# Kernel optimization log

Measured on AMD Instinct MI355X. Metric: run time of the kernel, lower is better.

The kernel has to match this reference:

```python
import jax, jax.numpy as jnp
import numpy as np

# B anchors, N neighbors, M views, F raw features, OBS router obs dim,
# D d_model, H heads, L layers, FF ffn dim, HID router hidden, OUT out_dim
B, N, M, F, OBS, D, H, L, FF, HID, OUT = 4096, 64, 4, 128, 64, 64, 4, 2, 128, 64, 8
EPS = 1e-6

def _ln(x, g, b):
    m = x.mean(-1, keepdims=True)
    v = ((x - m) ** 2).mean(-1, keepdims=True)
    return (x - m) / jnp.sqrt(v + 1e-5) * g + b

def _gelu(x):
    return jax.nn.gelu(x, approximate=False)

def setup_inputs() -> dict:
    key = jax.random.key(0)
    ks = iter(jax.random.split(key, 64))
    def nrm(shape, scale=0.05):
        return jax.random.normal(next(ks), shape, dtype=jnp.float32) * scale
    return dict(
        x_anc=jax.random.normal(next(ks), (B, F), dtype=jnp.float32),
        g_anc=jax.random.normal(next(ks), (B, OBS), dtype=jnp.float32),
        x_nei=jax.random.normal(next(ks), (B, N, F), dtype=jnp.float32),
        ew_anc=jax.random.uniform(next(ks), (B, N, M), dtype=jnp.float32),
        W_anc=nrm((F, D)), b_anc=jnp.zeros((D,), jnp.float32),
        Wv_emb=nrm((M, F, D)), bv_emb=jnp.zeros((M, D), jnp.float32),
        Wv_val=nrm((M, D, D)), bv_val=jnp.zeros((M, D), jnp.float32),
        r_Win=nrm((OBS + D, HID)), r_bin=jnp.zeros((HID,), jnp.float32),
        r_lng=jnp.ones((HID,), jnp.float32), r_lnb=jnp.zeros((HID,), jnp.float32),
        r_W1=nrm((HID, HID)), r_b1=jnp.zeros((HID,), jnp.float32),
        r_W2=nrm((HID, HID)), r_b2=jnp.zeros((HID,), jnp.float32),
        r_Wview=nrm((H, HID, M)), r_bview=jnp.zeros((H, M), jnp.float32),
        r_Wmode=nrm((H, HID)), r_bmode=jnp.zeros((H,), jnp.float32),
        log_tau=jnp.zeros((H,), jnp.float32),
        L_Wq=nrm((L, D, D)), L_Wk=nrm((L, D, D)), L_Wv=nrm((L, D, D)), L_Wo=nrm((L, D, D)),
        L_ln1g=jnp.ones((L, D), jnp.float32), L_ln1b=jnp.zeros((L, D), jnp.float32),
        L_ln2g=jnp.ones((L, D), jnp.float32), L_ln2b=jnp.zeros((L, D), jnp.float32),
        L_Wf1=nrm((L, D, FF)), L_bf1=jnp.zeros((L, FF), jnp.float32),
        L_Wf2=nrm((L, FF, D)), L_bf2=jnp.zeros((L, D), jnp.float32),
        p_lng=jnp.ones((D,), jnp.float32), p_lnb=jnp.zeros((D,), jnp.float32),
        p_W1=nrm((D, D // 2)), p_b1=jnp.zeros((D // 2,), jnp.float32),
        p_W2=nrm((D // 2, OUT)), p_b2=jnp.zeros((OUT,), jnp.float32),
    )

def reference(x_anc, g_anc, x_nei, ew_anc,
              W_anc, b_anc, Wv_emb, bv_emb, Wv_val, bv_val,
              r_Win, r_bin, r_lng, r_lnb, r_W1, r_b1, r_W2, r_b2,
              r_Wview, r_bview, r_Wmode, r_bmode, log_tau,
              L_Wq, L_Wk, L_Wv, L_Wo, L_ln1g, L_ln1b, L_ln2g, L_ln2b,
              L_Wf1, L_bf1, L_Wf2, L_bf2,
              p_lng, p_lnb, p_W1, p_b1, p_W2, p_b2):
    view_mask = (ew_anc > 0).astype(ew_anc.dtype)  # default view_mask
    # anchor / per-view neighbor embeddings
    h_anc = x_anc @ W_anc + b_anc                                    # [B,D]
    h_nei = jnp.einsum('bnf,mfd->bmnd', x_nei, Wv_emb) + bv_emb[None, :, None, :]  # [B,M,N,D]
    # per-view values + masked weight normalization + weighted neighbor sum
    vals = jnp.einsum('bmnd,mde->bmne', h_nei, Wv_val) + bv_val[None, :, None, :]
    w = (ew_anc * view_mask).transpose(0, 2, 1)                      # [B,M,N]
    w = w / jnp.clip(w.sum(-1, keepdims=True), EPS)
    per_view_ctx = jnp.einsum('bmn,bmnd->bmd', w, vals)              # [B,M,D]
    ctx_vec = per_view_ctx.mean(1)                                   # [B,D]
    iso_view_ctxs = per_view_ctx                                     # same masked reduce (no lbl_delta)
    # SplitTrackRouter
    h = jnp.concatenate([g_anc, ctx_vec], -1) @ r_Win + r_bin
    h = _gelu(_ln(h, r_lng, r_lnb))
    h = _gelu(h @ r_W1 + r_b1)
    h = _gelu(h @ r_W2 + r_b2)
    pi = jax.nn.softmax(jnp.einsum('bk,hkm->bhm', h, r_Wview) + r_bview, axis=-1)  # [B,H,M]
    beta = jax.nn.sigmoid(jnp.einsum('bk,hk->bh', h, r_Wmode) + r_bmode)           # [B,H]
    tau = jnp.exp(log_tau)                                                         # [H]
    iso_heads = jnp.einsum('bhm,bmd->bhd', pi, iso_view_ctxs)                      # [B,H,D]
    # SparseGeomLayer stack: anchor->neighbor cross attention gated by pi-weighted edge weights
    h_nei_shared = h_nei[:, 0]                                                     # [B,N,D]
    dh = D // H
    scale = 1.0 / (float(dh) ** 0.5)
    w_view = jnp.einsum('bhm,bnm->bhn', pi, ew_anc * view_mask)                    # [B,H,N]
    gate = jnp.log(w_view + EPS)
    x = h_anc
    for l in range(L):
        q = (x @ L_Wq[l]).reshape(B, H, dh)
        k = (h_nei_shared @ L_Wk[l]).reshape(B, N, H, dh)
        v = (h_nei_shared @ L_Wv[l]).reshape(B, N, H, dh)
        scores = jnp.einsum('bhd,bnhd->bhn', q, k) * scale / tau[None, :, None] + gate
        attn = jax.nn.softmax(scores, axis=-1)
        ctx = jnp.einsum('bhn,bnhd->bhd', attn, v).reshape(B, D) @ L_Wo[l]
        x = _ln(x + ctx, L_ln1g[l], L_ln1b[l])
        ff = _gelu(x @ L_Wf1[l] + L_bf1[l]) @ L_Wf2[l] + L_bf2[l]
        x = _ln(x + ff, L_ln2g[l], L_ln2b[l])
    # blend_iso_interaction
    blended = ((1.0 - beta)[..., None] * iso_heads + beta[..., None] * x[:, None, :]).mean(1)  # [B,D]
    # pred head
    y = _ln(blended, p_lng, p_lnb)
    y = _gelu(y @ p_W1 + p_b1) @ p_W2 + p_b2
    return y
```

## Files before the change

kernel.cpp:

```cpp
#include <hip/hip_runtime.h>
#include <hip/hip_bf16.h>
#include <math.h>

#define NB 4096
#define NN 64
#define NM 4
#define NF 128
#define NOBS 64
#define ND 64
#define NH 4
#define NLAYER 2
#define NFF 128
#define NHID 64
#define NOUT 8
#define EPSC 1e-6f

typedef unsigned short ushort_t;
typedef __attribute__((ext_vector_type(8))) short short8v;
typedef __attribute__((ext_vector_type(4))) float f32x4;

#define MFMA16(a, b, c) __builtin_amdgcn_mfma_f32_16x16x32_bf16((a), (b), (c), 0, 0, 0)

struct GParams {
    const float* x_anc; const float* g_anc; const float* x_nei; const float* ew_anc;
    const float* W_anc; const float* b_anc;
    const float* Wv_emb; const float* bv_emb; const float* Wv_val; const float* bv_val;
    const float* r_Win; const float* r_bin; const float* r_lng; const float* r_lnb;
    const float* r_W1; const float* r_b1; const float* r_W2; const float* r_b2;
    const float* r_Wview; const float* r_bview; const float* r_Wmode; const float* r_bmode;
    const float* log_tau;
    const float* L_Wq; const float* L_Wk; const float* L_Wv; const float* L_Wo;
    const float* L_ln1g; const float* L_ln1b; const float* L_ln2g; const float* L_ln2b;
    const float* L_Wf1; const float* L_bf1; const float* L_Wf2; const float* L_bf2;
    const float* p_lng; const float* p_lnb; const float* p_W1; const float* p_b1;
    const float* p_W2; const float* p_b2;
    const uint4* wsf;
    float* out;
};

__device__ __forceinline__ float gelu_f(float x) {
    return 0.5f * x * (1.0f + erff(x * 0.7071067811865476f));
}
__device__ __forceinline__ float wsum64(float v) {
#pragma unroll
    for (int off = 32; off > 0; off >>= 1) v += __shfl_xor(v, off, 64);
    return v;
}
__device__ __forceinline__ float wmax64(float v) {
#pragma unroll
    for (int off = 32; off > 0; off >>= 1) v = fmaxf(v, __shfl_xor(v, off, 64));
    return v;
}
__device__ __forceinline__ float bf2f(ushort_t u) {
    union { unsigned int i; float f; } c; c.i = ((unsigned int)u) << 16; return c.f;
}
__device__ __forceinline__ ushort_t f2bf(float f) {
    __hip_bfloat16 h = __float2bfloat16(f);
    ushort_t u; __builtin_memcpy(&u, &h, 2); return u;
}
__device__ __forceinline__ short8v ld_frag(const uint4* p) {
    union { uint4 q; short8v v; } u; u.q = *p; return u.v;
}

__global__ void prep_w(const float* Wv_emb, const float* L_Wk, const float* L_Wv, uint4* ws)
{
    int task = blockIdx.x * 256 + threadIdx.x;
    if (task >= 3072) return;
    int lane = task & 63;
    int frag = task >> 6;
    const float* src; int ks, ct; uint4 *dhi, *dlo;
    if (frag < 16) {
        ks = frag >> 2; ct = frag & 3;
        src = Wv_emb;
        dhi = ws + (size_t)frag * 64 + lane;
        dlo = ws + 1024 + (size_t)frag * 64 + lane;
    } else {
        int g = frag - 16;
        int matidx = g >> 3;
        int fi = g & 7;
        ks = fi >> 2; ct = fi & 3;
        src = ((matidx & 1) ? L_Wv : L_Wk) + (size_t)(matidx >> 1) * (ND * ND);
        dhi = ws + 2048 + (size_t)matidx * 1024 + (size_t)fi * 64 + lane;
        dlo = dhi + 512;
    }
    union { ushort_t u[8]; uint4 q; } hi, lo;
#pragma unroll
    for (int i = 0; i < 8; i++) {
        int k = ks * 32 + (lane >> 4) * 8 + i;
        int d = ct * 16 + (lane & 15);
        float w = src[k * ND + d];
        ushort_t h = f2bf(w);
        hi.u[i] = h;
        lo.u[i] = f2bf(w - bf2f(h));
    }
    *dhi = hi.q;
    *dlo = lo.q;
}

__global__ __launch_bounds__(256, 3)
void gora_fused(GParams P)
{
    const int b = blockIdx.x;
    const int t = threadIdx.x;
    const int lane = t & 63;
    const int wave = t >> 6;

    __shared__ alignas(16) char u1buf[NN * NF * 2];
    __shared__ float hv[NM][ND];
    __shared__ __hip_bfloat16 kb16[NN][ND + 2];
    __shared__ __hip_bfloat16 vb16[NN][ND + 2];
    __shared__ float ew_s[NN * NM];
    __shared__ float winv[NM], wssum[NM];
    __shared__ float xa[NF];
    __shared__ float ga[NOBS];
    __shared__ float xw[NM][NF];
    __shared__ float pvc[NM][ND];
    __shared__ float hfin[NHID];
    __shared__ float pi_raw[NH * NM];
    __shared__ float pi_s[NH][NM];
    __shared__ float beta_s[NH];
    __shared__ float gate_s[NH][NN];
    __shared__ float xcur[ND];
    __shared__ float qv[ND];
    __shared__ float attn_s[NH][NN];
    __shared__ float ctx_s[ND];
    __shared__ float ffs[NFF];
    __shared__ float sA[ND];
    __shared__ float sB[ND];

    {
        float e = P.ew_anc[(size_t)b * NN * NM + t];
        ew_s[t] = (e > 0.0f) ? e : 0.0f;
    }
    if (t < NF) xa[t] = P.x_anc[(size_t)b * NF + t];
    else if (t < NF + NOBS) ga[t - NF] = P.g_anc[(size_t)b * NOBS + (t - NF)];
    {
        const float4* xn4 = (const float4*)(P.x_nei + (size_t)b * NN * NF);
#pragma unroll
        for (int i = 0; i < 8; i++) {
            int i4 = t + i * 256;
            float4 v4 = xn4[i4];
            __hip_bfloat162 p0, p1;
            p0.x = __float2bfloat16(v4.x); p0.y = __float2bfloat16(v4.y);
            p1.x = __float2bfloat16(v4.z); p1.y = __float2bfloat16(v4.w);
            int n = i4 >> 5;
            int c = (i4 >> 1) & 15;
            char* dstb = u1buf + n * 256 + ((c ^ (n & 15)) << 4) + (i4 & 1) * 8;
            ((__hip_bfloat162*)dstb)[0] = p0;
            ((__hip_bfloat162*)dstb)[1] = p1;
        }
    }
    __syncthreads();

    if (t < NM) {
        float s = 0.0f;
        for (int n = 0; n < NN; n++) s += ew_s[n * NM + t];
        float c = fmaxf(s, EPSC);
        winv[t]  = 1.0f / c;
        wssum[t] = s / c;
    }
    if (t >= 64 && t < 128) {
        int d = t - 64;
        float acc = P.b_anc[d];
        for (int f = 0; f < NF; f++) acc += xa[f] * P.W_anc[f * ND + d];
        xcur[d] = acc;
    }
    __syncthreads();

    {
        int f = t & (NF - 1);
        int m0 = t >> 7;
        const char* base = u1buf + ((((f >> 3)) << 4)) * 0;
        float a0 = 0.f, a1 = 0.f;
        for (int n = 0; n < NN; n++) {
            const ushort_t* xp = (const ushort_t*)(u1buf + n * 256 + (((f >> 3) ^ (n & 15)) << 4) + (f & 7) * 2);
            float xv = bf2f(*xp);
            a0 += ew_s[n * NM + m0] * xv;
            a1 += ew_s[n * NM + m0 + 2] * xv;
        }
        xw[m0][f]     = a0 * winv[m0];
        xw[m0 + 2][f] = a1 * winv[m0 + 2];
    }

    short8v afr[4];
    {
        const int row = wave * 16 + (lane & 15);
        const int sub = lane >> 4;
#pragma unroll
        for (int ks = 0; ks < 4; ks++) {
            int c = ks * 4 + sub;
            afr[ks] = *(const short8v*)(u1buf + row * 256 + ((c ^ (row & 15)) << 4));
        }
    }
    __syncthreads();

    {
        const int n0 = wave * 16;
        const int colb = lane & 15;
        const int rsub = lane >> 4;
#pragma unroll
        for (int ct = 0; ct < 4; ct++) {
            float bias = P.bv_emb[ct * 16 + colb];
            f32x4 c = {bias, bias, bias, bias};
#pragma unroll
            for (int ks = 0; ks < 4; ks++) {
                short8v bhi = ld_frag(P.wsf + (size_t)(ks * 4 + ct) * 64 + lane);
                short8v blo = ld_frag(P.wsf + 1024 + (size_t)(ks * 4 + ct) * 64 + lane);
                c = MFMA16(afr[ks], bhi, c);
                c = MFMA16(afr[ks], blo, c);
            }
#pragma unroll
            for (int e = 0; e < 4; e++) {
                int n = n0 + rsub * 4 + e;
                int d = ct * 16 + colb;
                *(float*)(u1buf + n * 256 + ((((d >> 2) ^ (n & 15))) << 4) + (d & 3) * 4) = c[e];
            }
        }
    }

    {
        int m = wave, d = lane;
        float acc = wssum[m] * P.bv_emb[m * ND + d];
        const float* We = P.Wv_emb + (size_t)m * NF * ND;
        for (int f = 0; f < NF; f++) acc += xw[m][f] * We[f * ND + d];
        hv[m][d] = acc;
    }
    __syncthreads();
    {
        int m = wave, d = lane;
        float acc = wssum[m] * P.bv_val[m * ND + d];
        const float* Wv = P.Wv_val + (size_t)m * ND * ND;
        for (int k = 0; k < ND; k++) acc += hv[m][k] * Wv[k * ND + d];
        pvc[m][d] = acc;
    }
    __syncthreads();

    if (t < ND) sA[t] = 0.25f * (pvc[0][t] + pvc[1][t] + pvc[2][t] + pvc[3][t]);
    __syncthreads();
    if (t < NHID) {
        float acc = P.r_bin[t];
        for (int f = 0; f < NOBS; f++) acc += ga[f] * P.r_Win[f * NHID + t];
        for (int f = 0; f < ND;   f++) acc += sA[f] * P.r_Win[(NOBS + f) * NHID + t];
        float mean = wsum64(acc) * (1.0f / 64.0f);
        float dv = acc - mean;
        float var = wsum64(dv * dv) * (1.0f / 64.0f);
        float xln = dv * rsqrtf(var + 1e-5f) * P.r_lng[t] + P.r_lnb[t];
        sB[t] = gelu_f(xln);
    }
    __syncthreads();
    if (t < NHID) {
        float acc = P.r_b1[t];
        for (int k = 0; k < NHID; k++) acc += sB[k] * P.r_W1[k * NHID + t];
        sA[t] = gelu_f(acc);
    }
    __syncthreads();
    if (t < NHID) {
        float acc = P.r_b2[t];
        for (int k = 0; k < NHID; k++) acc += sA[k] * P.r_W2[k * NHID + t];
        hfin[t] = gelu_f(acc);
    }
    __syncthreads();

    if (t < NH * NM) {
        int h = t >> 2, mm = t & 3;
        float acc = P.r_bview[h * NM + mm];
        for (int k = 0; k < NHID; k++) acc += hfin[k] * P.r_Wview[(h * NHID + k) * NM + mm];
        pi_raw[t] = acc;
    }
    if (t >= 64 && t < 64 + NH) {
        int h = t - 64;
        float acc = P.r_bmode[h];
        for (int k = 0; k < NHID; k++) acc += hfin[k] * P.r_Wmode[h * NHID + k];
        beta_s[h] = 1.0f / (1.0f + expf(-acc));
    }
    __syncthreads();
    if (t < NH) {
        float mx = -1e30f;
        for (int mm = 0; mm < NM; mm++) mx = fmaxf(mx, pi_raw[t * NM + mm]);
        float s = 0.f, e[NM];
        for (int mm = 0; mm < NM; mm++) { e[mm] = expf(pi_raw[t * NM + mm] - mx); s += e[mm]; }
        for (int mm = 0; mm < NM; mm++) pi_s[t][mm] = e[mm] / s;
    }
    __syncthreads();

    {
        int h = wave, n = lane;
        float wv = 0.f;
        for (int mm = 0; mm < NM; mm++) wv += pi_s[h][mm] * ew_s[n * NM + mm];
        gate_s[h][n] = logf(wv + EPSC);
    }
    __syncthreads();

    const float inv_tau_scale = 0.25f / expf(P.log_tau[wave]);
    for (int l = 0; l < NLAYER; l++) {
        const float* Wq  = P.L_Wq  + l * ND * ND;
        const float* Wo  = P.L_Wo  + l * ND * ND;
        const float* ln1g = P.L_ln1g + l * ND;
        const float* ln1b = P.L_ln1b + l * ND;
        const float* ln2g = P.L_ln2g + l * ND;
        const float* ln2b = P.L_ln2b + l * ND;
        const float* Wf1 = P.L_Wf1 + l * ND * NFF;
        const float* bf1 = P.L_bf1 + l * NFF;
        const float* Wf2 = P.L_Wf2 + l * NFF * ND;
        const float* bf2 = P.L_bf2 + l * ND;

        if (t < ND) {
            float acc = 0.f;
            for (int k = 0; k < ND; k++) acc += xcur[k] * Wq[k * ND + t];
            qv[t] = acc;
        }
        {
            const int n0 = wave * 16;
            const int row = n0 + (lane & 15);
            const int rsub = lane >> 4;
            short8v ahi[2], alo[2];
#pragma unroll
            for (int ks = 0; ks < 2; ks++) {
                int c0 = ks * 8 + rsub * 2;
                f32x4 x0 = *(const f32x4*)(u1buf + row * 256 + ((c0 ^ (row & 15)) << 4));
                f32x4 x1 = *(const f32x4*)(u1buf + row * 256 + (((c0 + 1) ^ (row & 15)) << 4));
                union { ushort_t u[8]; short8v v; } uh, ul;
#pragma unroll
                for (int i = 0; i < 8; i++) {
                    float w = (i < 4) ? x0[i] : x1[i - 4];
                    ushort_t h = f2bf(w);
                    uh.u[i] = h;
                    ul.u[i] = f2bf(w - bf2f(h));
                }
                ahi[ks] = uh.v; alo[ks] = ul.v;
            }
            const uint4* bbase = P.wsf + 2048 + (size_t)(l * 2) * 1024;
#pragma unroll
            for (int mat = 0; mat < 2; mat++) {
                const uint4* bb = bbase + (size_t)mat * 1024;
                __hip_bfloat16* dst = mat ? &vb16[0][0] : &kb16[0][0];
#pragma unroll
                for (int ct = 0; ct < 4; ct++) {
                    f32x4 c = {0.f, 0.f, 0.f, 0.f};
#pragma unroll
                    for (int ks = 0; ks < 2; ks++) {
                        short8v bhi = ld_frag(bb + (size_t)(ks * 4 + ct) * 64 + lane);
                        short8v blo = ld_frag(bb + 512 + (size_t)(ks * 4 + ct) * 64 + lane);
                        c = MFMA16(ahi[ks], bhi, c);
                        c = MFMA16(ahi[ks], blo, c);
                        c = MFMA16(alo[ks], bhi, c);
                    }
#pragma unroll
                    for (int e = 0; e < 4; e++) {
                        int n = n0 + rsub * 4 + e;
                        dst[n * (ND + 2) + ct * 16 + (lane & 15)] = __float2bfloat16(c[e]);
                    }
                }
            }
        }
        __syncthreads();
        {
            int h = wave, n = lane;
            float s = 0.f;
#pragma unroll
            for (int j = 0; j < 16; j++)
                s += qv[h * 16 + j] * __bfloat162float(kb16[n][h * 16 + j]);
            s = s * inv_tau_scale + gate_s[h][n];
            float mx = wmax64(s);
            float e = expf(s - mx);
            float se = wsum64(e);
            attn_s[h][n] = e / se;
        }
        __syncthreads();
        if (t < ND) {
            int h = t >> 4;
            float acc = 0.f;
            for (int n = 0; n < NN; n++) acc += attn_s[h][n] * __bfloat162float(vb16[n][t]);
            ctx_s[t] = acc;
        }
        __syncthreads();
        if (t < ND) {
            float acc = 0.f;
            for (int c = 0; c < ND; c++) acc += ctx_s[c] * Wo[c * ND + t];
            float xv = xcur[t] + acc;
            float mean = wsum64(xv) * (1.0f / 64.0f);
            float dv = xv - mean;
            float var = wsum64(dv * dv) * (1.0f / 64.0f);
            xcur[t] = dv * rsqrtf(var + 1e-5f) * ln1g[t] + ln1b[t];
        }
        __syncthreads();
        if (t < NFF) {
            float acc = bf1[t];
            for (int d = 0; d < ND; d++) acc += xcur[d] * Wf1[d * NFF + t];
            ffs[t] = gelu_f(acc);
        }
        __syncthreads();
        if (t < ND) {
            float acc = bf2[t];
            for (int j = 0; j < NFF; j++) acc += ffs[j] * Wf2[j * ND + t];
            float xv = xcur[t] + acc;
            float mean = wsum64(xv) * (1.0f / 64.0f);
            float dv = xv - mean;
            float var = wsum64(dv * dv) * (1.0f / 64.0f);
            xcur[t] = dv * rsqrtf(var + 1e-5f) * ln2g[t] + ln2b[t];
        }
        __syncthreads();
    }

    if (t < ND) {
        float acc = 0.f;
#pragma unroll
        for (int h = 0; h < NH; h++) {
            float iso = 0.f;
#pragma unroll
            for (int mm = 0; mm < NM; mm++) iso += pi_s[h][mm] * pvc[mm][t];
            acc += (1.0f - beta_s[h]) * iso + beta_s[h] * xcur[t];
        }
        float bl = acc * 0.25f;
        float mean = wsum64(bl) * (1.0f / 64.0f);
        float dv = bl - mean;
        float var = wsum64(dv * dv) * (1.0f / 64.0f);
        sA[t] = dv * rsqrtf(var + 1e-5f) * P.p_lng[t] + P.p_lnb[t];
    }
    __syncthreads();
    if (t < 32) {
        float acc = P.p_b1[t];
        for (int d = 0; d < ND; d++) acc += sA[d] * P.p_W1[d * 32 + t];
        sB[t] = gelu_f(acc);
    }
    __syncthreads();
    if (t < NOUT) {
        float acc = P.p_b2[t];
        for (int j = 0; j < 32; j++) acc += sB[j] * P.p_W2[j * NOUT + t];
        P.out[(size_t)b * NOUT + t] = acc;
    }
}

extern "C" void kernel_launch(void* const* d_in, const int* in_sizes, int n_in,
                              void* d_out, int out_size, void* d_ws, size_t ws_size,
                              hipStream_t stream)
{
    (void)in_sizes; (void)n_in; (void)ws_size; (void)out_size;
    GParams P;
    P.x_anc   = (const float*)d_in[0];
    P.g_anc   = (const float*)d_in[1];
    P.x_nei   = (const float*)d_in[2];
    P.ew_anc  = (const float*)d_in[3];
    P.W_anc   = (const float*)d_in[4];
    P.b_anc   = (const float*)d_in[5];
    P.Wv_emb  = (const float*)d_in[6];
    P.bv_emb  = (const float*)d_in[7];
    P.Wv_val  = (const float*)d_in[8];
    P.bv_val  = (const float*)d_in[9];
    P.r_Win   = (const float*)d_in[10];
    P.r_bin   = (const float*)d_in[11];
    P.r_lng   = (const float*)d_in[12];
    P.r_lnb   = (const float*)d_in[13];
    P.r_W1    = (const float*)d_in[14];
    P.r_b1    = (const float*)d_in[15];
    P.r_W2    = (const float*)d_in[16];
    P.r_b2    = (const float*)d_in[17];
    P.r_Wview = (const float*)d_in[18];
    P.r_bview = (const float*)d_in[19];
    P.r_Wmode = (const float*)d_in[20];
    P.r_bmode = (const float*)d_in[21];
    P.log_tau = (const float*)d_in[22];
    P.L_Wq    = (const float*)d_in[23];
    P.L_Wk    = (const float*)d_in[24];
    P.L_Wv    = (const float*)d_in[25];
    P.L_Wo    = (const float*)d_in[26];
    P.L_ln1g  = (const float*)d_in[27];
    P.L_ln1b  = (const float*)d_in[28];
    P.L_ln2g  = (const float*)d_in[29];
    P.L_ln2b  = (const float*)d_in[30];
    P.L_Wf1   = (const float*)d_in[31];
    P.L_bf1   = (const float*)d_in[32];
    P.L_Wf2   = (const float*)d_in[33];
    P.L_bf2   = (const float*)d_in[34];
    P.p_lng   = (const float*)d_in[35];
    P.p_lnb   = (const float*)d_in[36];
    P.p_W1    = (const float*)d_in[37];
    P.p_b1    = (const float*)d_in[38];
    P.p_W2    = (const float*)d_in[39];
    P.p_b2    = (const float*)d_in[40];
    P.wsf     = (const uint4*)d_ws;
    P.out     = (float*)d_out;
    hipLaunchKernelGGL(prep_w, dim3(12), dim3(256), 0, stream,
                       P.Wv_emb, P.L_Wk, P.L_Wv, (uint4*)d_ws);
    hipLaunchKernelGGL(gora_fused, dim3(NB), dim3(256), 0, stream, P);
}
```

Measured before the change: 447.1 us.

## Split serial small matvecs across all four waves with partial-sum reductions

Many small per-anchor GEMVs (anchor embedding, router MLP, Q projection, attention context, Wo, FFN layers, prediction head) previously ran on only one wave, each thread walking a long serial K loop. They are now split along K across all four waves, or across lanes with shuffle reductions. Partial sums go through new shared buffers and are combined in a following step. Some loops also get dual accumulators to break FMA dependency chains. This adds barriers and shared memory (which may lower occupancy) in exchange for shorter serial critical paths.

```diff
diff --git a/kernel.cpp b/kernel.cpp
--- a/kernel.cpp
+++ b/kernel.cpp
@@ -123,10 +123,12 @@
     __shared__ float xcur[ND];
     __shared__ float qv[ND];
     __shared__ float attn_s[NH][NN];
-    __shared__ float ctx_s[ND];
     __shared__ float ffs[NFF];
     __shared__ float sA[ND];
     __shared__ float sB[ND];
+    __shared__ float part_a[4][ND];
+    __shared__ float part_b[4][ND];
+    __shared__ float part_c[4][ND];
 
     {
         float e = P.ew_anc[(size_t)b * NN * NM + t];
@@ -159,24 +161,31 @@
         winv[t]  = 1.0f / c;
         wssum[t] = s / c;
     }
-    if (t >= 64 && t < 128) {
-        int d = t - 64;
-        float acc = P.b_anc[d];
-        for (int f = 0; f < NF; f++) acc += xa[f] * P.W_anc[f * ND + d];
-        xcur[d] = acc;
+    {
+        const float* Wr = P.W_anc + (wave * 32) * ND + lane;
+        float a0 = 0.f, a1 = 0.f;
+#pragma unroll
+        for (int f = 0; f < 32; f += 2) {
+            a0 += xa[wave * 32 + f] * Wr[f * ND];
+            a1 += xa[wave * 32 + f + 1] * Wr[(f + 1) * ND];
+        }
+        part_a[wave][lane] = a0 + a1;
     }
     __syncthreads();
 
     {
         int f = t & (NF - 1);
         int m0 = t >> 7;
-        const char* base = u1buf + ((((f >> 3)) << 4)) * 0;
+        const int fc = f >> 3, fe = (f & 7) * 2;
         float a0 = 0.f, a1 = 0.f;
         for (int n = 0; n < NN; n++) {
-            const ushort_t* xp = (const ushort_t*)(u1buf + n * 256 + (((f >> 3) ^ (n & 15)) << 4) + (f & 7) * 2);
+            const ushort_t* xp = (const ushort_t*)(u1buf + n * 256 + ((fc ^ (n & 15)) << 4) + fe);
             float xv = bf2f(*xp);
-            a0 += ew_s[n * NM + m0] * xv;
-            a1 += ew_s[n * NM + m0 + 2] * xv;
+            float4 e4 = *(const float4*)&ew_s[n * NM];
+            float e0 = m0 ? e4.y : e4.x;
+            float e1 = m0 ? e4.w : e4.z;
+            a0 += e0 * xv;
+            a1 += e1 * xv;
         }
         xw[m0][f]     = a0 * winv[m0];
         xw[m0 + 2][f] = a1 * winv[m0 + 2];
@@ -220,27 +229,47 @@
 
     {
         int m = wave, d = lane;
-        float acc = wssum[m] * P.bv_emb[m * ND + d];
+        float a0 = wssum[m] * P.bv_emb[m * ND + d], a1 = 0.f;
         const float* We = P.Wv_emb + (size_t)m * NF * ND;
-        for (int f = 0; f < NF; f++) acc += xw[m][f] * We[f * ND + d];
-        hv[m][d] = acc;
+        for (int f = 0; f < NF; f += 2) {
+            a0 += xw[m][f] * We[f * ND + d];
+            a1 += xw[m][f + 1] * We[(f + 1) * ND + d];
+        }
+        hv[m][d] = a0 + a1;
     }
     __syncthreads();
     {
         int m = wave, d = lane;
-        float acc = wssum[m] * P.bv_val[m * ND + d];
+        float a0 = wssum[m] * P.bv_val[m * ND + d], a1 = 0.f;
         const float* Wv = P.Wv_val + (size_t)m * ND * ND;
-        for (int k = 0; k < ND; k++) acc += hv[m][k] * Wv[k * ND + d];
-        pvc[m][d] = acc;
-    }
-    __syncthreads();
-
-    if (t < ND) sA[t] = 0.25f * (pvc[0][t] + pvc[1][t] + pvc[2][t] + pvc[3][t]);
+        for (int k = 0; k < ND; k += 2) {
+            a0 += hv[m][k] * Wv[k * ND + d];
+            a1 += hv[m][k + 1] * Wv[(k + 1) * ND + d];
+        }
+        pvc[m][d] = a0 + a1;
+    }
+    __syncthreads();
+
+    if (t < ND) {
+        sA[t] = 0.25f * (pvc[0][t] + pvc[1][t] + pvc[2][t] + pvc[3][t]);
+        xcur[t] = P.b_anc[t] + part_a[0][t] + part_a[1][t] + part_a[2][t] + part_a[3][t];
+    }
+    __syncthreads();
+
+    {
+        const float* xin = (wave < 2) ? (ga + wave * 32) : (sA + (wave - 2) * 32);
+        const float* Wr = P.r_Win + (wave * 32) * NHID + lane;
+        float a0 = 0.f, a1 = 0.f;
+#pragma unroll
+        for (int i = 0; i < 32; i += 2) {
+            a0 += xin[i] * Wr[i * NHID];
+            a1 += xin[i + 1] * Wr[(i + 1) * NHID];
+        }
+        part_a[wave][lane] = a0 + a1;
+    }
     __syncthreads();
     if (t < NHID) {
-        float acc = P.r_bin[t];
-        for (int f = 0; f < NOBS; f++) acc += ga[f] * P.r_Win[f * NHID + t];
-        for (int f = 0; f < ND;   f++) acc += sA[f] * P.r_Win[(NOBS + f) * NHID + t];
+        float acc = P.r_bin[t] + part_a[0][t] + part_a[1][t] + part_a[2][t] + part_a[3][t];
         float mean = wsum64(acc) * (1.0f / 64.0f);
         float dv = acc - mean;
         float var = wsum64(dv * dv) * (1.0f / 64.0f);
@@ -248,17 +277,27 @@
         sB[t] = gelu_f(xln);
     }
     __syncthreads();
-    if (t < NHID) {
-        float acc = P.r_b1[t];
-        for (int k = 0; k < NHID; k++) acc += sB[k] * P.r_W1[k * NHID + t];
-        sA[t] = gelu_f(acc);
-    }
-    __syncthreads();
-    if (t < NHID) {
-        float acc = P.r_b2[t];
-        for (int k = 0; k < NHID; k++) acc += sA[k] * P.r_W2[k * NHID + t];
-        hfin[t] = gelu_f(acc);
-    }
+    {
+        const float* Wr = P.r_W1 + (wave * 16) * NHID + lane;
+        float acc = 0.f;
+#pragma unroll
+        for (int i = 0; i < 16; i++) acc += sB[wave * 16 + i] * Wr[i * NHID];
+        part_a[wave][lane] = acc;
+    }
+    __syncthreads();
+    if (t < NHID)
+        sA[t] = gelu_f(P.r_b1[t] + part_a[0][t] + part_a[1][t] + part_a[2][t] + part_a[3][t]);
+    __syncthreads();
+    {
+        const float* Wr = P.r_W2 + (wave * 16) * NHID + lane;
+        float acc = 0.f;
+#pragma unroll
+        for (int i = 0; i < 16; i++) acc += sA[wave * 16 + i] * Wr[i * NHID];
+        part_a[wave][lane] = acc;
+    }
+    __syncthreads();
+    if (t < NHID)
+        hfin[t] = gelu_f(P.r_b2[t] + part_a[0][t] + part_a[1][t] + part_a[2][t] + part_a[3][t]);
     __syncthreads();
 
     if (t < NH * NM) {
@@ -304,10 +343,17 @@
         const float* Wf2 = P.L_Wf2 + l * NFF * ND;
         const float* bf2 = P.L_bf2 + l * ND;
 
-        if (t < ND) {
+        {
+            int j = lane >> 2, kc = lane & 3;
             float acc = 0.f;
-            for (int k = 0; k < ND; k++) acc += xcur[k] * Wq[k * ND + t];
-            qv[t] = acc;
+#pragma unroll
+            for (int i = 0; i < 16; i++) {
+                int k = kc * 16 + i;
+                acc += xcur[k] * Wq[k * ND + wave * 16 + j];
+            }
+            acc += __shfl_xor(acc, 1, 64);
+            acc += __shfl_xor(acc, 2, 64);
+            if (kc == 0) qv[wave * 16 + j] = acc;
         }
         {
             const int n0 = wave * 16;
@@ -367,33 +413,63 @@
             attn_s[h][n] = e / se;
         }
         __syncthreads();
+        {
+            int d = lane, h = d >> 4;
+            float acc = 0.f;
+#pragma unroll
+            for (int i = 0; i < 16; i++) {
+                int n = wave * 16 + i;
+                acc += attn_s[h][n] * __bfloat162float(vb16[n][d]);
+            }
+            part_b[wave][d] = acc;
+        }
+        __syncthreads();
+        {
+            int d = lane;
+            float acc = 0.f;
+#pragma unroll
+            for (int i = 0; i < 16; i++) {
+                int c = wave * 16 + i;
+                float ctxc = part_b[0][c] + part_b[1][c] + part_b[2][c] + part_b[3][c];
+                acc += ctxc * Wo[c * ND + d];
+            }
+            part_c[wave][d] = acc;
+        }
+        __syncthreads();
         if (t < ND) {
-            int h = t >> 4;
-            float acc = 0.f;
-            for (int n = 0; n < NN; n++) acc += attn_s[h][n] * __bfloat162float(vb16[n][t]);
-            ctx_s[t] = acc;
-        }
-        __syncthreads();
-        if (t < ND) {
-            float acc = 0.f;
-            for (int c = 0; c < ND; c++) acc += ctx_s[c] * Wo[c * ND + t];
-            float xv = xcur[t] + acc;
+            float xv = xcur[t] + part_c[0][t] + part_c[1][t] + part_c[2][t] + part_c[3][t];
             float mean = wsum64(xv) * (1.0f / 64.0f);
             float dv = xv - mean;
             float var = wsum64(dv * dv) * (1.0f / 64.0f);
             xcur[t] = dv * rsqrtf(var + 1e-5f) * ln1g[t] + ln1b[t];
         }
         __syncthreads();
-        if (t < NFF) {
-            float acc = bf1[t];
-            for (int d = 0; d < ND; d++) acc += xcur[d] * Wf1[d * NFF + t];
-            ffs[t] = gelu_f(acc);
+        {
+            int j = t >> 1, kh = t & 1;
+            float acc = 0.f;
+#pragma unroll
+            for (int i = 0; i < 32; i++) {
+                int d = kh * 32 + i;
+                acc += xcur[d] * Wf1[d * NFF + j];
+            }
+            acc += __shfl_xor(acc, 1, 64);
+            if (kh == 0) ffs[j] = gelu_f(acc + bf1[j]);
+        }
+        __syncthreads();
+        {
+            int d = lane;
+            const float* Wr = Wf2 + (wave * 32) * ND + d;
+            float a0 = 0.f, a1 = 0.f;
+#pragma unroll
+            for (int i = 0; i < 32; i += 2) {
+                a0 += ffs[wave * 32 + i] * Wr[i * ND];
+                a1 += ffs[wave * 32 + i + 1] * Wr[(i + 1) * ND];
+            }
+            part_b[wave][d] = a0 + a1;
         }
         __syncthreads();
         if (t < ND) {
-            float acc = bf2[t];
-            for (int j = 0; j < NFF; j++) acc += ffs[j] * Wf2[j * ND + t];
-            float xv = xcur[t] + acc;
+            float xv = xcur[t] + bf2[t] + part_b[0][t] + part_b[1][t] + part_b[2][t] + part_b[3][t];
             float mean = wsum64(xv) * (1.0f / 64.0f);
             float dv = xv - mean;
             float var = wsum64(dv * dv) * (1.0f / 64.0f);
@@ -418,16 +494,32 @@
         sA[t] = dv * rsqrtf(var + 1e-5f) * P.p_lng[t] + P.p_lnb[t];
     }
     __syncthreads();
+    {
+        int o = lane & 31;
+        int kp = wave * 2 + (lane >> 5);
+        const float* Wr = P.p_W1 + (kp * 8) * 32 + o;
+        float acc = 0.f;
+#pragma unroll
+        for (int i = 0; i < 8; i++) acc += sA[kp * 8 + i] * Wr[i * 32];
+        ((float*)part_b)[kp * 32 + o] = acc;
+    }
+    __syncthreads();
     if (t < 32) {
         float acc = P.p_b1[t];
-        for (int d = 0; d < ND; d++) acc += sA[d] * P.p_W1[d * 32 + t];
+#pragma unroll
+        for (int kp = 0; kp < 8; kp++) acc += ((float*)part_b)[kp * 32 + t];
         sB[t] = gelu_f(acc);
     }
     __syncthreads();
-    if (t < NOUT) {
-        float acc = P.p_b2[t];
-        for (int j = 0; j < 32; j++) acc += sB[j] * P.p_W2[j * NOUT + t];
-        P.out[(size_t)b * NOUT + t] = acc;
+    if (t < NOUT * 8) {
+        int o = t >> 3, kc = t & 7;
+        float acc = 0.f;
+#pragma unroll
+        for (int i = 0; i < 4; i++) acc += sB[kc * 4 + i] * P.p_W2[(kc * 4 + i) * NOUT + o];
+        acc += __shfl_xor(acc, 1, 64);
+        acc += __shfl_xor(acc, 2, 64);
+        acc += __shfl_xor(acc, 4, 64);
+        if (kc == 0) P.out[(size_t)b * NOUT + o] = acc + P.p_b2[o];
     }
 }
 
```

After: 525.7 us. +17.6%, slower.
